# Kernel tuning notes

Hardware: AMD Instinct MI355X
Metric: run time of the kernel (lower is better)

Reference implementation:

```python
import jax, jax.numpy as jnp
import numpy as np

D = 4096      # per-region feature dim (input_feature_dims)
OBJ = 20      # regions per frame (memory row = 20*4096)
M = 1000      # temporal_mem_size
K = 1         # temporal_K


def l2norm(x, axis=-1, eps=1e-12):
    # torch F.normalize: x / clamp_min(||x||, eps)
    n = jnp.linalg.norm(x, axis=axis, keepdims=True)
    return x / jnp.maximum(n, eps)


def setup_inputs() -> dict:
    key = jax.random.key(0)
    k1, k2, k3, k4, k5 = jax.random.split(key, 5)
    B, Q, F_ = 4, 4, 20
    return {
        "QR_frm_weight_p": jax.random.normal(k1, (B, Q, F_), jnp.float32),
        "input_pos_feature": jax.random.normal(k2, (B, F_, OBJ, D), jnp.float32),
        "mem1": jax.random.normal(k3, (M, OBJ * D), jnp.float32),
        "mem2": jax.random.normal(k4, (M, OBJ * D), jnp.float32),
        "rand_idx": jax.random.randint(k5, (B, Q, K), 0, F_ - K),
    }


def reference(QR_frm_weight_p, input_pos_feature, mem1, mem2, rand_idx):
    B, Q, F_ = QR_frm_weight_p.shape

    # top-K high-attention frames and a random low-attention frame per query
    _, high_idx = jax.lax.top_k(QR_frm_weight_p, K)              # [B,Q,K]
    _, low_all = jax.lax.top_k(-QR_frm_weight_p, F_ - K)         # smallest, asc
    low_idx = jnp.take_along_axis(low_all, rand_idx, axis=-1)    # [B,Q,K]

    # CVPR feature branch: L2-normalize region features
    R = l2norm(input_pos_feature)                                # [B,F,OBJ,D]

    # max-pool over regions, L2-normalize, then nearest memory slot
    R_max = l2norm(jnp.max(R, axis=2).reshape(-1, D))            # [B*F, D]
    mem1_mp = l2norm(jnp.max(mem1.reshape(M, OBJ, D), axis=1))   # [M, D]
    mem2_mp = l2norm(jnp.max(mem2.reshape(M, OBJ, D), axis=1))   # [M, D]
    sim1 = jnp.argmax(R_max @ mem1_mp.T, axis=-1)                # [B*F]
    Rp_updated = mem1[sim1].reshape(B, F_, OBJ, D)
    sim2 = jnp.argmax(R_max @ mem2_mp.T, axis=-1)
    Rn_updated = mem2[sim2].reshape(B, F_, OBJ, D)

    b_ix = jnp.arange(B)[:, None, None]                          # [B,1,1]
    q_ix = jnp.arange(Q)[None, :, None]                          # [1,Q,1]

    # gather selected frames: [B,Q,K,OBJ,D] -> [Q,B,K,OBJ,D]
    R_high = jnp.transpose(R[b_ix, high_idx], (1, 0, 2, 3, 4))
    R_low = jnp.transpose(R[b_ix, low_idx], (1, 0, 2, 3, 4))

    # Rn: copy of R per query, high-attention frames replaced by mem2
    # counterfactuals gathered at LOW indices (as in the torch code, where
    # `splits` still holds the low-region splits at that point).
    Rn = jnp.broadcast_to(R[:, None], (B, Q, F_, OBJ, D))
    Rn = Rn.at[b_ix, q_ix, high_idx].set(Rn_updated[b_ix, low_idx])
    Rn = jnp.transpose(Rn, (1, 0, 2, 3, 4))                      # [Q,B,F,OBJ,D]

    # Rp: low-attention frames replaced by mem1 entries at low indices
    Rp = jnp.broadcast_to(R[:, None], (B, Q, F_, OBJ, D))
    Rp = Rp.at[b_ix, q_ix, low_idx].set(Rp_updated[b_ix, low_idx])
    Rp = jnp.transpose(Rp, (1, 0, 2, 3, 4))                      # [Q,B,F,OBJ,D]

    # nearest-memory assignment for selected high/low frames
    R_high_mp = l2norm(jnp.max(R_high.reshape(-1, OBJ, D), axis=1))
    R_low_mp = l2norm(jnp.max(R_low.reshape(-1, OBJ, D), axis=1))
    high_sim = jnp.argmax(R_high_mp @ mem2_mp.T, axis=-1)        # [Q*B*K]
    low_sim = jnp.argmax(R_low_mp @ mem1_mp.T, axis=-1)

    return Rp, Rn, high_sim, low_sim
```

## Files before the change

### kernel.cpp

```cpp
#include <hip/hip_runtime.h>

#define D 4096
#define OBJ 20
#define M_MEM 1000
#define F_ 20
#define FRAME_F4 20480
#define RP_SZ 26214400
#define OUT_TAIL 52428800

__device__ __forceinline__ float4 f4max(float4 a, float4 b){
  return make_float4(fmaxf(a.x,b.x), fmaxf(a.y,b.y), fmaxf(a.z,b.z), fmaxf(a.w,b.w));
}
__device__ __forceinline__ float4 f4scale(float4 a, float s){
  return make_float4(a.x*s, a.y*s, a.z*s, a.w*s);
}
__device__ __forceinline__ double f4ss(float4 a){
  return (double)a.x*a.x + (double)a.y*a.y + (double)a.z*a.z + (double)a.w*a.w;
}

__device__ __forceinline__ unsigned int fkey(float f){
  unsigned int b = __float_as_uint(f);
  return (b & 0x80000000u) ? ~b : (b | 0x80000000u);
}

__device__ __forceinline__ double blockReduce256(double v){
  #pragma unroll
  for (int off = 32; off > 0; off >>= 1) v += __shfl_down(v, off, 64);
  __shared__ double sh[4];
  int w = threadIdx.x >> 6;
  if ((threadIdx.x & 63) == 0) sh[w] = v;
  __syncthreads();
  return sh[0] + sh[1] + sh[2] + sh[3];
}

__global__ void k_norms(const float* __restrict__ x, float* __restrict__ inv_norm){
  int row = blockIdx.x;
  const float4* p = (const float4*)x + (size_t)row * 1024;
  double ss = 0.0;
  for (int i = threadIdx.x; i < 1024; i += 256){ float4 v = __ldg(p + i); ss += f4ss(v); }
  ss = blockReduce256(ss);
  if (threadIdx.x == 0) inv_norm[row] = (float)(1.0 / fmax(sqrt(ss), 1e-12));
}

__global__ void k_rmax(const float* __restrict__ x, const float* __restrict__ inv_norm,
                       float* __restrict__ rmaxn){
  int bf = blockIdx.x;
  __shared__ float sinv[OBJ];
  if (threadIdx.x < OBJ) sinv[threadIdx.x] = inv_norm[bf*OBJ + threadIdx.x];
  __syncthreads();
  float4 mv[4];
  #pragma unroll
  for (int i = 0; i < 4; i++) mv[i] = make_float4(-INFINITY,-INFINITY,-INFINITY,-INFINITY);
  const float4* base = (const float4*)x + (size_t)bf * OBJ * 1024;
  for (int o = 0; o < OBJ; o++){
    float s = sinv[o];
    const float4* p = base + o*1024;
    #pragma unroll
    for (int i = 0; i < 4; i++){
      float4 v = __ldg(p + threadIdx.x + i*256);
      mv[i] = f4max(mv[i], f4scale(v, s));
    }
  }
  double ss = 0.0;
  #pragma unroll
  for (int i = 0; i < 4; i++) ss += f4ss(mv[i]);
  ss = blockReduce256(ss);
  float rinv = (float)(1.0 / fmax(sqrt(ss), 1e-12));
  float4* outp = (float4*)rmaxn + (size_t)bf * 1024;
  #pragma unroll
  for (int i = 0; i < 4; i++) outp[threadIdx.x + i*256] = f4scale(mv[i], rinv);
}

__global__ void k_memmp(const float* __restrict__ mem1, const float* __restrict__ mem2,
                        float* __restrict__ out1, float* __restrict__ out2){
  int blk = blockIdx.x;
  const float* mem; float* outp; int m;
  if (blk < M_MEM){ mem = mem1; outp = out1; m = blk; }
  else            { mem = mem2; outp = out2; m = blk - M_MEM; }
  const float4* base = (const float4*)mem + (size_t)m * FRAME_F4;
  float4 mv[4];
  #pragma unroll
  for (int i = 0; i < 4; i++) mv[i] = make_float4(-INFINITY,-INFINITY,-INFINITY,-INFINITY);
  for (int o = 0; o < OBJ; o++){
    const float4* p = base + o*1024;
    #pragma unroll
    for (int i = 0; i < 4; i++) mv[i] = f4max(mv[i], __ldg(p + threadIdx.x + i*256));
  }
  double ss = 0.0;
  #pragma unroll
  for (int i = 0; i < 4; i++) ss += f4ss(mv[i]);
  ss = blockReduce256(ss);
  float rinv = (float)(1.0 / fmax(sqrt(ss), 1e-12));
  float4* o4 = (float4*)outp + (size_t)m * 1024;
  #pragma unroll
  for (int i = 0; i < 4; i++) o4[threadIdx.x + i*256] = f4scale(mv[i], rinv);
}

__global__ void k_sel(const float* __restrict__ qr, const int* __restrict__ rand_idx,
                      int* __restrict__ high_idx, int* __restrict__ low_idx,
                      unsigned long long* __restrict__ packed){
  int t = threadIdx.x;
  if (t < 160) packed[t] = 0ull;
  if (t >= 16) return;
  float w[F_];
  for (int f = 0; f < F_; f++) w[f] = qr[t*F_ + f];
  int hi = 0; float hv = w[0];
  for (int f = 1; f < F_; f++) if (w[f] > hv){ hv = w[f]; hi = f; }
  int r = rand_idx[t];
  bool used[F_];
  for (int f = 0; f < F_; f++) used[f] = false;
  used[hi] = true;
  int li = 0;
  for (int it = 0; it <= r; it++){
    int bi = -1; float bv = INFINITY;
    for (int f = 0; f < F_; f++) if (!used[f] && w[f] < bv){ bv = w[f]; bi = f; }
    used[bi] = true; li = bi;
  }
  high_idx[t] = hi; low_idx[t] = li;
}

__global__ void k_dots(const float* __restrict__ mpn1, const float* __restrict__ mpn2,
                       const float* __restrict__ rmaxn,
                       unsigned long long* __restrict__ packed){
  int blk = blockIdx.x;
  int which = blk / 250;
  int chunk = blk % 250;
  const float* mpn = which ? mpn2 : mpn1;
  __shared__ float4 rows[4*1024];
  __shared__ float pv[4][80];
  const float4* src = (const float4*)mpn + (size_t)chunk * 4 * 1024;
  for (int i = threadIdx.x; i < 4096; i += 256) rows[i] = __ldg(src + i);
  __syncthreads();
  int w = threadIdx.x >> 6, lane = threadIdx.x & 63;
  const float4* mrow = rows + w*1024;
  for (int bf = 0; bf < 80; bf++){
    const float4* rrow = (const float4*)rmaxn + (size_t)bf * 1024;
    float ax = 0.f, ay = 0.f, az = 0.f, aw = 0.f;
    #pragma unroll
    for (int i = 0; i < 16; i++){
      float4 r = __ldg(rrow + i*64 + lane);
      float4 m = mrow[i*64 + lane];
      ax += r.x*m.x; ay += r.y*m.y; az += r.z*m.z; aw += r.w*m.w;
    }
    float s = (ax + ay) + (az + aw);
    #pragma unroll
    for (int off = 32; off > 0; off >>= 1) s += __shfl_down(s, off, 64);
    if (lane == 0) pv[w][bf] = s;
  }
  __syncthreads();
  if (threadIdx.x < 80){
    int bf = threadIdx.x;
    float best = pv[0][bf]; int bw = 0;
    #pragma unroll
    for (int w2 = 1; w2 < 4; w2++){ float v = pv[w2][bf]; if (v > best){ best = v; bw = w2; } }
    unsigned long long pk = ((unsigned long long)fkey(best) << 32) |
                            (unsigned int)(chunk*4 + bw);
    atomicMax(packed + which*80 + bf, pk);
  }
}

__global__ void k_fin(const unsigned long long* __restrict__ packed,
                      const int* __restrict__ high_idx, const int* __restrict__ low_idx,
                      int* __restrict__ rp_row, int* __restrict__ rn_row,
                      float* __restrict__ outp){
  int t = threadIdx.x;
  if (t >= 16) return;
  int b = t >> 2, q = t & 3;
  int hi = high_idx[t], lo = low_idx[t];
  int sim1_lo = (int)(unsigned int)packed[      b*F_ + lo];
  int sim2_lo = (int)(unsigned int)packed[80 + b*F_ + lo];
  int sim2_hi = (int)(unsigned int)packed[80 + b*F_ + hi];
  rp_row[t] = sim1_lo;
  rn_row[t] = sim2_lo;
  outp[OUT_TAIL      + q*4 + b] = (float)sim2_hi;
  outp[OUT_TAIL + 16 + q*4 + b] = (float)sim1_lo;
}

__global__ void k_write(const float* __restrict__ x, const float* __restrict__ inv_norm,
                        const float* __restrict__ mem1, const float* __restrict__ mem2,
                        const int* __restrict__ high_idx, const int* __restrict__ low_idx,
                        const int* __restrict__ rp_row, const int* __restrict__ rn_row,
                        float* __restrict__ outp){
  int bid = blockIdx.x;
  int fid = bid >> 3;
  int part = bid & 7;
  int q = fid / 80;
  int rem = fid % 80;
  int b = rem / F_;
  int f = rem % F_;
  int t16 = b*4 + q;
  int lo = __ldg(low_idx + t16), hi = __ldg(high_idx + t16);
  bool isLo = (f == lo), isHi = (f == hi);
  const float4* xf   = (const float4*)x + (size_t)(b*F_ + f)*FRAME_F4;
  const float*  invn = inv_norm + (b*F_ + f)*OBJ;
  const float4* m1p  = (const float4*)mem1 + (size_t)__ldg(rp_row + t16)*FRAME_F4;
  const float4* m2p  = (const float4*)mem2 + (size_t)__ldg(rn_row + t16)*FRAME_F4;
  float4* o4 = (float4*)outp;
  size_t fbase = (size_t)fid * FRAME_F4;
  #pragma unroll
  for (int k = 0; k < 10; k++){
    int e4 = part*2560 + k*256 + threadIdx.x;
    int o = e4 >> 10;
    float s = __ldg(invn + o);
    float4 xn = f4scale(__ldg(xf + e4), s);
    float4 rp = isLo ? __ldg(m1p + e4) : xn;
    float4 rn = isHi ? __ldg(m2p + e4) : xn;
    o4[fbase + e4] = rp;
    o4[(RP_SZ/4) + fbase + e4] = rn;
  }
}

extern "C" void kernel_launch(void* const* d_in, const int* in_sizes, int n_in,
                              void* d_out, int out_size, void* d_ws, size_t ws_size,
                              hipStream_t stream) {
  const float* qr       = (const float*)d_in[0];
  const float* x        = (const float*)d_in[1];
  const float* mem1     = (const float*)d_in[2];
  const float* mem2     = (const float*)d_in[3];
  const int*   rand_idx = (const int*)  d_in[4];
  float* outp = (float*)d_out;

  float* mpn1     = (float*)d_ws;
  float* mpn2     = mpn1 + 4096000;
  float* rmaxn    = mpn2 + 4096000;
  float* inv_norm = rmaxn + 327680;
  unsigned long long* packed = (unsigned long long*)(inv_norm + 1600);
  int*   high_idx = (int*)(packed + 160);
  int*   low_idx  = high_idx + 16;
  int*   rp_row   = low_idx + 16;
  int*   rn_row   = rp_row + 16;

  k_norms<<<1600, 256, 0, stream>>>(x, inv_norm);
  k_memmp<<<2000, 256, 0, stream>>>(mem1, mem2, mpn1, mpn2);
  k_rmax <<<80,   256, 0, stream>>>(x, inv_norm, rmaxn);
  k_sel  <<<1,    192, 0, stream>>>(qr, rand_idx, high_idx, low_idx, packed);
  k_dots <<<500,  256, 0, stream>>>(mpn1, mpn2, rmaxn, packed);
  k_fin  <<<1,    64,  0, stream>>>(packed, high_idx, low_idx, rp_row, rn_row, outp);
  k_write<<<2560, 256, 0, stream>>>(x, inv_norm, mem1, mem2, high_idx, low_idx,
                                    rp_row, rn_row, outp);
}
```

Before: 934.0 us.

## Fuse preprocessing kernels, restructure memory dot products, use nontemporal streaming stores

Merges the norm, region max-pool, memory max-pool and selection kernels into one launch dispatched by block index, and folds the finalize step into the write kernel. The dot-product kernel now has each wavefront score all four memory rows against one query row, so each query row is read once per block instead of four times and the shared-memory reduction pass goes away. The write kernel branches per frame so that only the needed memory row is read, caches per-region inverse norms in shared memory, and uses nontemporal loads and stores for the large streaming traffic. The cost is more launch-time divergence and less independence between stages.

```diff
diff --git a/kernel.cpp b/kernel.cpp
--- a/kernel.cpp
+++ b/kernel.cpp
@@ -5,8 +5,10 @@
 #define M_MEM 1000
 #define F_ 20
 #define FRAME_F4 20480
-#define RP_SZ 26214400
+#define RP_F4 6553600
 #define OUT_TAIL 52428800
+
+typedef float vf4 __attribute__((ext_vector_type(4)));
 
 __device__ __forceinline__ float4 f4max(float4 a, float4 b){
   return make_float4(fmaxf(a.x,b.x), fmaxf(a.y,b.y), fmaxf(a.z,b.z), fmaxf(a.w,b.w));
@@ -16,6 +18,14 @@
 }
 __device__ __forceinline__ double f4ss(float4 a){
   return (double)a.x*a.x + (double)a.y*a.y + (double)a.z*a.z + (double)a.w*a.w;
+}
+__device__ __forceinline__ void ntst(float4* p, float4 v){
+  vf4 t; t.x = v.x; t.y = v.y; t.z = v.z; t.w = v.w;
+  __builtin_nontemporal_store(t, (vf4*)p);
+}
+__device__ __forceinline__ float4 ntld(const float4* p){
+  vf4 t = __builtin_nontemporal_load((const vf4*)p);
+  return make_float4(t.x, t.y, t.z, t.w);
 }
 
 __device__ __forceinline__ unsigned int fkey(float f){
@@ -33,90 +43,93 @@
   return sh[0] + sh[1] + sh[2] + sh[3];
 }
 
-__global__ void k_norms(const float* __restrict__ x, float* __restrict__ inv_norm){
-  int row = blockIdx.x;
-  const float4* p = (const float4*)x + (size_t)row * 1024;
-  double ss = 0.0;
-  for (int i = threadIdx.x; i < 1024; i += 256){ float4 v = __ldg(p + i); ss += f4ss(v); }
-  ss = blockReduce256(ss);
-  if (threadIdx.x == 0) inv_norm[row] = (float)(1.0 / fmax(sqrt(ss), 1e-12));
-}
-
-__global__ void k_rmax(const float* __restrict__ x, const float* __restrict__ inv_norm,
-                       float* __restrict__ rmaxn){
-  int bf = blockIdx.x;
-  __shared__ float sinv[OBJ];
-  if (threadIdx.x < OBJ) sinv[threadIdx.x] = inv_norm[bf*OBJ + threadIdx.x];
-  __syncthreads();
-  float4 mv[4];
-  #pragma unroll
-  for (int i = 0; i < 4; i++) mv[i] = make_float4(-INFINITY,-INFINITY,-INFINITY,-INFINITY);
-  const float4* base = (const float4*)x + (size_t)bf * OBJ * 1024;
-  for (int o = 0; o < OBJ; o++){
-    float s = sinv[o];
-    const float4* p = base + o*1024;
-    #pragma unroll
-    for (int i = 0; i < 4; i++){
-      float4 v = __ldg(p + threadIdx.x + i*256);
-      mv[i] = f4max(mv[i], f4scale(v, s));
-    }
-  }
-  double ss = 0.0;
-  #pragma unroll
-  for (int i = 0; i < 4; i++) ss += f4ss(mv[i]);
-  ss = blockReduce256(ss);
-  float rinv = (float)(1.0 / fmax(sqrt(ss), 1e-12));
-  float4* outp = (float4*)rmaxn + (size_t)bf * 1024;
-  #pragma unroll
-  for (int i = 0; i < 4; i++) outp[threadIdx.x + i*256] = f4scale(mv[i], rinv);
-}
-
-__global__ void k_memmp(const float* __restrict__ mem1, const float* __restrict__ mem2,
-                        float* __restrict__ out1, float* __restrict__ out2){
+__global__ void k_fused1(const float* __restrict__ x,
+                         const float* __restrict__ mem1, const float* __restrict__ mem2,
+                         const float* __restrict__ qr, const int* __restrict__ rand_idx,
+                         float* __restrict__ mpn1, float* __restrict__ mpn2,
+                         float* __restrict__ rmaxn, float* __restrict__ inv_norm,
+                         unsigned long long* __restrict__ packed,
+                         int* __restrict__ high_idx, int* __restrict__ low_idx){
   int blk = blockIdx.x;
-  const float* mem; float* outp; int m;
-  if (blk < M_MEM){ mem = mem1; outp = out1; m = blk; }
-  else            { mem = mem2; outp = out2; m = blk - M_MEM; }
-  const float4* base = (const float4*)mem + (size_t)m * FRAME_F4;
-  float4 mv[4];
-  #pragma unroll
-  for (int i = 0; i < 4; i++) mv[i] = make_float4(-INFINITY,-INFINITY,-INFINITY,-INFINITY);
-  for (int o = 0; o < OBJ; o++){
-    const float4* p = base + o*1024;
-    #pragma unroll
-    for (int i = 0; i < 4; i++) mv[i] = f4max(mv[i], __ldg(p + threadIdx.x + i*256));
-  }
-  double ss = 0.0;
-  #pragma unroll
-  for (int i = 0; i < 4; i++) ss += f4ss(mv[i]);
-  ss = blockReduce256(ss);
-  float rinv = (float)(1.0 / fmax(sqrt(ss), 1e-12));
-  float4* o4 = (float4*)outp + (size_t)m * 1024;
-  #pragma unroll
-  for (int i = 0; i < 4; i++) o4[threadIdx.x + i*256] = f4scale(mv[i], rinv);
-}
-
-__global__ void k_sel(const float* __restrict__ qr, const int* __restrict__ rand_idx,
-                      int* __restrict__ high_idx, int* __restrict__ low_idx,
-                      unsigned long long* __restrict__ packed){
-  int t = threadIdx.x;
-  if (t < 160) packed[t] = 0ull;
-  if (t >= 16) return;
-  float w[F_];
-  for (int f = 0; f < F_; f++) w[f] = qr[t*F_ + f];
-  int hi = 0; float hv = w[0];
-  for (int f = 1; f < F_; f++) if (w[f] > hv){ hv = w[f]; hi = f; }
-  int r = rand_idx[t];
-  bool used[F_];
-  for (int f = 0; f < F_; f++) used[f] = false;
-  used[hi] = true;
-  int li = 0;
-  for (int it = 0; it <= r; it++){
-    int bi = -1; float bv = INFINITY;
-    for (int f = 0; f < F_; f++) if (!used[f] && w[f] < bv){ bv = w[f]; bi = f; }
-    used[bi] = true; li = bi;
-  }
-  high_idx[t] = hi; low_idx[t] = li;
+  int tid = threadIdx.x;
+  if (blk >= 80 && blk < 2080){
+    int id = blk - 80;
+    const float* mem; float* outp; int m;
+    if (id < M_MEM){ mem = mem1; outp = mpn1; m = id; }
+    else           { mem = mem2; outp = mpn2; m = id - M_MEM; }
+    const float4* base = (const float4*)mem + (size_t)m * FRAME_F4;
+    float4 mv[4];
+    #pragma unroll
+    for (int i = 0; i < 4; i++) mv[i] = make_float4(-INFINITY,-INFINITY,-INFINITY,-INFINITY);
+    for (int o = 0; o < OBJ; o++){
+      const float4* p = base + o*1024;
+      #pragma unroll
+      for (int i = 0; i < 4; i++) mv[i] = f4max(mv[i], ntld(p + tid + i*256));
+    }
+    double ss = 0.0;
+    #pragma unroll
+    for (int i = 0; i < 4; i++) ss += f4ss(mv[i]);
+    ss = blockReduce256(ss);
+    float rinv = (float)(1.0 / fmax(sqrt(ss), 1e-12));
+    float4* o4 = (float4*)outp + (size_t)m * 1024;
+    #pragma unroll
+    for (int i = 0; i < 4; i++) o4[tid + i*256] = f4scale(mv[i], rinv);
+  } else if (blk < 80){
+    __shared__ float sinv[OBJ];
+    int w = tid >> 6, lane = tid & 63;
+    const float4* base = (const float4*)x + (size_t)blk * FRAME_F4;
+    for (int o = w*5; o < w*5 + 5; o++){
+      const float4* p = base + o*1024;
+      double ss = 0.0;
+      #pragma unroll
+      for (int j = 0; j < 16; j++) ss += f4ss(__ldg(p + j*64 + lane));
+      #pragma unroll
+      for (int off = 32; off > 0; off >>= 1) ss += __shfl_down(ss, off, 64);
+      if (lane == 0){
+        float inv = (float)(1.0 / fmax(sqrt(ss), 1e-12));
+        sinv[o] = inv;
+        inv_norm[blk*OBJ + o] = inv;
+      }
+    }
+    __syncthreads();
+    float4 mv[4];
+    #pragma unroll
+    for (int i = 0; i < 4; i++) mv[i] = make_float4(-INFINITY,-INFINITY,-INFINITY,-INFINITY);
+    for (int o = 0; o < OBJ; o++){
+      float s = sinv[o];
+      const float4* p = base + o*1024;
+      #pragma unroll
+      for (int i = 0; i < 4; i++) mv[i] = f4max(mv[i], f4scale(__ldg(p + tid + i*256), s));
+    }
+    double ss = 0.0;
+    #pragma unroll
+    for (int i = 0; i < 4; i++) ss += f4ss(mv[i]);
+    ss = blockReduce256(ss);
+    float rinv = (float)(1.0 / fmax(sqrt(ss), 1e-12));
+    float4* outp = (float4*)rmaxn + (size_t)blk * 1024;
+    #pragma unroll
+    for (int i = 0; i < 4; i++) outp[tid + i*256] = f4scale(mv[i], rinv);
+  } else {
+    int t = tid;
+    if (t < 160) packed[t] = 0ull;
+    if (t < 16){
+      float wv[F_];
+      for (int f = 0; f < F_; f++) wv[f] = qr[t*F_ + f];
+      int hi = 0; float hv = wv[0];
+      for (int f = 1; f < F_; f++) if (wv[f] > hv){ hv = wv[f]; hi = f; }
+      int r = rand_idx[t];
+      bool used[F_];
+      for (int f = 0; f < F_; f++) used[f] = false;
+      used[hi] = true;
+      int li = 0;
+      for (int it = 0; it <= r; it++){
+        int bi = -1; float bv = INFINITY;
+        for (int f = 0; f < F_; f++) if (!used[f] && wv[f] < bv){ bv = wv[f]; bi = f; }
+        used[bi] = true; li = bi;
+      }
+      high_idx[t] = hi; low_idx[t] = li;
+    }
+  }
 }
 
 __global__ void k_dots(const float* __restrict__ mpn1, const float* __restrict__ mpn2,
@@ -127,86 +140,109 @@
   int chunk = blk % 250;
   const float* mpn = which ? mpn2 : mpn1;
   __shared__ float4 rows[4*1024];
-  __shared__ float pv[4][80];
-  const float4* src = (const float4*)mpn + (size_t)chunk * 4 * 1024;
+  const float4* src = (const float4*)mpn + (size_t)chunk * 4096;
   for (int i = threadIdx.x; i < 4096; i += 256) rows[i] = __ldg(src + i);
   __syncthreads();
   int w = threadIdx.x >> 6, lane = threadIdx.x & 63;
-  const float4* mrow = rows + w*1024;
-  for (int bf = 0; bf < 80; bf++){
+  unsigned long long* slot = packed + which*80;
+  for (int bf = w; bf < 80; bf += 4){
     const float4* rrow = (const float4*)rmaxn + (size_t)bf * 1024;
-    float ax = 0.f, ay = 0.f, az = 0.f, aw = 0.f;
+    float d0 = 0.f, d1 = 0.f, d2 = 0.f, d3 = 0.f;
     #pragma unroll
     for (int i = 0; i < 16; i++){
-      float4 r = __ldg(rrow + i*64 + lane);
-      float4 m = mrow[i*64 + lane];
-      ax += r.x*m.x; ay += r.y*m.y; az += r.z*m.z; aw += r.w*m.w;
-    }
-    float s = (ax + ay) + (az + aw);
-    #pragma unroll
-    for (int off = 32; off > 0; off >>= 1) s += __shfl_down(s, off, 64);
-    if (lane == 0) pv[w][bf] = s;
-  }
-  __syncthreads();
-  if (threadIdx.x < 80){
-    int bf = threadIdx.x;
-    float best = pv[0][bf]; int bw = 0;
-    #pragma unroll
-    for (int w2 = 1; w2 < 4; w2++){ float v = pv[w2][bf]; if (v > best){ best = v; bw = w2; } }
-    unsigned long long pk = ((unsigned long long)fkey(best) << 32) |
-                            (unsigned int)(chunk*4 + bw);
-    atomicMax(packed + which*80 + bf, pk);
-  }
-}
-
-__global__ void k_fin(const unsigned long long* __restrict__ packed,
-                      const int* __restrict__ high_idx, const int* __restrict__ low_idx,
-                      int* __restrict__ rp_row, int* __restrict__ rn_row,
-                      float* __restrict__ outp){
-  int t = threadIdx.x;
-  if (t >= 16) return;
-  int b = t >> 2, q = t & 3;
-  int hi = high_idx[t], lo = low_idx[t];
-  int sim1_lo = (int)(unsigned int)packed[      b*F_ + lo];
-  int sim2_lo = (int)(unsigned int)packed[80 + b*F_ + lo];
-  int sim2_hi = (int)(unsigned int)packed[80 + b*F_ + hi];
-  rp_row[t] = sim1_lo;
-  rn_row[t] = sim2_lo;
-  outp[OUT_TAIL      + q*4 + b] = (float)sim2_hi;
-  outp[OUT_TAIL + 16 + q*4 + b] = (float)sim1_lo;
+      float4 r  = __ldg(rrow + i*64 + lane);
+      float4 m0 = rows[       i*64 + lane];
+      float4 m1 = rows[1024 + i*64 + lane];
+      float4 m2 = rows[2048 + i*64 + lane];
+      float4 m3 = rows[3072 + i*64 + lane];
+      d0 += r.x*m0.x + r.y*m0.y + r.z*m0.z + r.w*m0.w;
+      d1 += r.x*m1.x + r.y*m1.y + r.z*m1.z + r.w*m1.w;
+      d2 += r.x*m2.x + r.y*m2.y + r.z*m2.z + r.w*m2.w;
+      d3 += r.x*m3.x + r.y*m3.y + r.z*m3.z + r.w*m3.w;
+    }
+    #pragma unroll
+    for (int off = 32; off > 0; off >>= 1){
+      d0 += __shfl_down(d0, off, 64);
+      d1 += __shfl_down(d1, off, 64);
+      d2 += __shfl_down(d2, off, 64);
+      d3 += __shfl_down(d3, off, 64);
+    }
+    if (lane == 0){
+      float best = d0; int bi = 0;
+      if (d1 > best){ best = d1; bi = 1; }
+      if (d2 > best){ best = d2; bi = 2; }
+      if (d3 > best){ best = d3; bi = 3; }
+      unsigned long long pk = ((unsigned long long)fkey(best) << 32) |
+                              (unsigned int)(chunk*4 + bi);
+      atomicMax(slot + bf, pk);
+    }
+  }
 }
 
 __global__ void k_write(const float* __restrict__ x, const float* __restrict__ inv_norm,
                         const float* __restrict__ mem1, const float* __restrict__ mem2,
                         const int* __restrict__ high_idx, const int* __restrict__ low_idx,
-                        const int* __restrict__ rp_row, const int* __restrict__ rn_row,
+                        const unsigned long long* __restrict__ packed,
                         float* __restrict__ outp){
   int bid = blockIdx.x;
+  int tid = threadIdx.x;
   int fid = bid >> 3;
   int part = bid & 7;
   int q = fid / 80;
-  int rem = fid % 80;
+  int rem = fid - q*80;
   int b = rem / F_;
-  int f = rem % F_;
+  int f = rem - b*F_;
   int t16 = b*4 + q;
   int lo = __ldg(low_idx + t16), hi = __ldg(high_idx + t16);
-  bool isLo = (f == lo), isHi = (f == hi);
-  const float4* xf   = (const float4*)x + (size_t)(b*F_ + f)*FRAME_F4;
-  const float*  invn = inv_norm + (b*F_ + f)*OBJ;
-  const float4* m1p  = (const float4*)mem1 + (size_t)__ldg(rp_row + t16)*FRAME_F4;
-  const float4* m2p  = (const float4*)mem2 + (size_t)__ldg(rn_row + t16)*FRAME_F4;
+
+  if (bid == 0 && tid < 16){
+    int tb = tid >> 2, tq = tid & 3;
+    int thi = __ldg(high_idx + tid), tlo = __ldg(low_idx + tid);
+    int s2hi = (int)(unsigned int)__ldg(packed + 80 + tb*F_ + thi);
+    int s1lo = (int)(unsigned int)__ldg(packed +      tb*F_ + tlo);
+    outp[OUT_TAIL      + tq*4 + tb] = (float)s2hi;
+    outp[OUT_TAIL + 16 + tq*4 + tb] = (float)s1lo;
+  }
+
+  __shared__ float sinv[OBJ];
+  if (tid < OBJ) sinv[tid] = inv_norm[(b*F_ + f)*OBJ + tid];
+  __syncthreads();
+
+  const float4* xf = (const float4*)x + (size_t)(b*F_ + f)*FRAME_F4;
   float4* o4 = (float4*)outp;
   size_t fbase = (size_t)fid * FRAME_F4;
-  #pragma unroll
-  for (int k = 0; k < 10; k++){
-    int e4 = part*2560 + k*256 + threadIdx.x;
-    int o = e4 >> 10;
-    float s = __ldg(invn + o);
-    float4 xn = f4scale(__ldg(xf + e4), s);
-    float4 rp = isLo ? __ldg(m1p + e4) : xn;
-    float4 rn = isHi ? __ldg(m2p + e4) : xn;
-    o4[fbase + e4] = rp;
-    o4[(RP_SZ/4) + fbase + e4] = rn;
+
+  if (f == lo){
+    int rpRow = (int)(unsigned int)__ldg(packed + b*F_ + lo);
+    const float4* m1p = (const float4*)mem1 + (size_t)rpRow * FRAME_F4;
+    #pragma unroll
+    for (int k = 0; k < 10; k++){
+      int e4 = part*2560 + k*256 + tid;
+      float s = sinv[(part*10 + k) >> 2];
+      float4 xn = f4scale(__ldg(xf + e4), s);
+      ntst(o4 + fbase + e4, __ldg(m1p + e4));
+      ntst(o4 + RP_F4 + fbase + e4, xn);
+    }
+  } else if (f == hi){
+    int rnRow = (int)(unsigned int)__ldg(packed + 80 + b*F_ + lo);
+    const float4* m2p = (const float4*)mem2 + (size_t)rnRow * FRAME_F4;
+    #pragma unroll
+    for (int k = 0; k < 10; k++){
+      int e4 = part*2560 + k*256 + tid;
+      float s = sinv[(part*10 + k) >> 2];
+      float4 xn = f4scale(__ldg(xf + e4), s);
+      ntst(o4 + fbase + e4, xn);
+      ntst(o4 + RP_F4 + fbase + e4, __ldg(m2p + e4));
+    }
+  } else {
+    #pragma unroll
+    for (int k = 0; k < 10; k++){
+      int e4 = part*2560 + k*256 + tid;
+      float s = sinv[(part*10 + k) >> 2];
+      float4 xn = f4scale(__ldg(xf + e4), s);
+      ntst(o4 + fbase + e4, xn);
+      ntst(o4 + RP_F4 + fbase + e4, xn);
+    }
   }
 }
 
@@ -227,15 +263,11 @@
   unsigned long long* packed = (unsigned long long*)(inv_norm + 1600);
   int*   high_idx = (int*)(packed + 160);
   int*   low_idx  = high_idx + 16;
-  int*   rp_row   = low_idx + 16;
-  int*   rn_row   = rp_row + 16;
-
-  k_norms<<<1600, 256, 0, stream>>>(x, inv_norm);
-  k_memmp<<<2000, 256, 0, stream>>>(mem1, mem2, mpn1, mpn2);
-  k_rmax <<<80,   256, 0, stream>>>(x, inv_norm, rmaxn);
-  k_sel  <<<1,    192, 0, stream>>>(qr, rand_idx, high_idx, low_idx, packed);
-  k_dots <<<500,  256, 0, stream>>>(mpn1, mpn2, rmaxn, packed);
-  k_fin  <<<1,    64,  0, stream>>>(packed, high_idx, low_idx, rp_row, rn_row, outp);
-  k_write<<<2560, 256, 0, stream>>>(x, inv_norm, mem1, mem2, high_idx, low_idx,
-                                    rp_row, rn_row, outp);
-}
+
+  k_fused1<<<2081, 256, 0, stream>>>(x, mem1, mem2, qr, rand_idx,
+                                     mpn1, mpn2, rmaxn, inv_norm,
+                                     packed, high_idx, low_idx);
+  k_dots  <<<500,  256, 0, stream>>>(mpn1, mpn2, rmaxn, packed);
+  k_write <<<2560, 256, 0, stream>>>(x, inv_norm, mem1, mem2,
+                                     high_idx, low_idx, packed, outp);
+}
```

Result: slower. 1.085 ms (+16.1%).
